# Kernel tuning notes

Hardware: AMD Instinct MI355X
Metric: run time of the kernel (lower is better)

Reference implementation:

```python
import math
import jax, jax.numpy as jnp
import numpy as np

B, S, D, H, HD = 2, 2048, 1024, 16, 64  # batch, seq, dim, heads, head_dim
EPS = 1e-5

def setup_inputs() -> dict:
    key = jax.random.key(0)
    ks = jax.random.split(key, 10)
    init = lambda k, shape: jax.random.normal(k, shape, jnp.float32) * 0.02
    return {
        "x": jax.random.normal(ks[0], (B, S, D), jnp.float32),
        "cos": jax.random.uniform(ks[1], (1, S, 1, 1, HD), dtype=jnp.float32),
        "sin": jax.random.uniform(ks[2], (1, S, 1, 1, HD), dtype=jnp.float32),
        "c": jax.random.normal(ks[3], (B, D), jnp.float32),
        "norm1_w": jnp.ones((D,), jnp.float32),
        "w_qkv": init(ks[4], (3 * D, D)),
        "w_out": init(ks[5], (D, D)),
        "norm2_w": jnp.ones((D,), jnp.float32),
        "mlp_w1": init(ks[6], (4 * D, D)),
        "mlp_b1": jnp.zeros((4 * D,), jnp.float32),
        "mlp_w2": init(ks[7], (D, 4 * D)),
        "mlp_b2": jnp.zeros((D,), jnp.float32),
        "ada_w": init(ks[8], (6 * D, D)),
        "ada_b": init(ks[9], (6 * D,)),
    }

def _ln(x, w):
    # LayerNorm computed in fp32, no bias, then scaled by weight
    xf = x.astype(jnp.float32)
    mu = xf.mean(-1, keepdims=True)
    var = xf.var(-1, keepdims=True)
    return (xf - mu) * jax.lax.rsqrt(var + EPS) * w

def _modulate(h, shift, scale):
    return h * (1.0 + scale[:, None, :]) + shift[:, None, :]

def reference(x, cos, sin, c, norm1_w, w_qkv, w_out, norm2_w,
              mlp_w1, mlp_b1, mlp_w2, mlp_b2, ada_w, ada_b):
    # adaLN modulation params: [B, 6D] -> six [B, D] chunks
    ada = c @ ada_w.T + ada_b
    sh_msa, sc_msa, g_msa, sh_mlp, sc_mlp, g_mlp = jnp.split(ada, 6, axis=-1)

    # attention branch (flash_attn path: no rotary applied, naive full softmax)
    h = _modulate(_ln(x, norm1_w), sh_msa, sc_msa)
    qkv = (h @ w_qkv.T).reshape(B, S, 3, H, HD)
    q, k, v = qkv[:, :, 0], qkv[:, :, 1], qkv[:, :, 2]
    scores = jnp.einsum('bqhd,bkhd->bhqk', q, k) / math.sqrt(HD)
    probs = jax.nn.softmax(scores, axis=-1)
    attn = jnp.einsum('bhqk,bkhd->bqhd', probs, v).reshape(B, S, D)
    # gate * dropout(out) + residual; eval mode -> dropout = identity
    x = x + g_msa[:, None, :] * (attn @ w_out.T)

    # MLP branch
    h = _modulate(_ln(x, norm2_w), sh_mlp, sc_mlp)
    h = jax.nn.gelu(h @ mlp_w1.T + mlp_b1, approximate=True) @ mlp_w2.T + mlp_b2
    return x + g_mlp[:, None, :] * h
```

## Files before the change

### kernel.cpp

```cpp
#include <hip/hip_runtime.h>
#include <stdint.h>

typedef __attribute__((ext_vector_type(4))) float f32x4;
typedef __attribute__((ext_vector_type(8))) __bf16 bf16x8;

#define DEV static __device__ __forceinline__

DEV unsigned short f2bf(float f){
    uint32_t u = __float_as_uint(f);
    u += 0x7FFFu + ((u >> 16) & 1u);
    return (unsigned short)(u >> 16);
}
DEV float bf2f(unsigned short s){
    uint32_t u = ((uint32_t)s) << 16;
    return __uint_as_float(u);
}

typedef __attribute__((address_space(1))) const void as1v;
typedef __attribute__((address_space(3))) void as3v;
DEV void g2l16(const void* g, void* l){
    __builtin_amdgcn_global_load_lds((as1v*)g, (as3v*)l, 16, 0, 0);
}

__global__ __launch_bounds__(256) void k_cast_bf16(const float* __restrict__ in,
                                                   unsigned short* __restrict__ out, int n4){
    int i = blockIdx.x * 256 + threadIdx.x;
    if (i < n4){
        float4 v = ((const float4*)in)[i];
        ((ushort4*)out)[i] = make_ushort4(f2bf(v.x), f2bf(v.y), f2bf(v.z), f2bf(v.w));
    }
}

__global__ __launch_bounds__(256) void k_cast_bf16q(const float* __restrict__ in,
                                                    unsigned short* __restrict__ out,
                                                    int n4, int nq4){
    int i = blockIdx.x * 256 + threadIdx.x;
    if (i < n4){
        float4 v = ((const float4*)in)[i];
        float s = (i < nq4) ? 0.18033688011112043f : 1.f;
        ((ushort4*)out)[i] = make_ushort4(f2bf(v.x * s), f2bf(v.y * s), f2bf(v.z * s), f2bf(v.w * s));
    }
}

__global__ __launch_bounds__(256) void k_ada(const float* __restrict__ c,
                                             const float* __restrict__ aw,
                                             const float* __restrict__ ab,
                                             float* __restrict__ out){
    int wid  = blockIdx.x * 4 + (threadIdx.x >> 6);
    int lane = threadIdx.x & 63;
    int b = wid / 6144, r = wid % 6144;
    const float4* cw = (const float4*)(c + (size_t)b * 1024);
    const float4* wr = (const float4*)(aw + (size_t)r * 1024);
    float s = 0.f;
    #pragma unroll
    for (int i = 0; i < 4; i++){
        float4 a = wr[lane + i * 64];
        float4 q = cw[lane + i * 64];
        s += a.x*q.x + a.y*q.y + a.z*q.z + a.w*q.w;
    }
    #pragma unroll
    for (int off = 32; off > 0; off >>= 1) s += __shfl_down(s, off);
    if (lane == 0) out[wid] = s + ab[r];
}

__global__ __launch_bounds__(256) void k_ln_mod(const float* __restrict__ x,
                                                const float* __restrict__ w,
                                                const float* __restrict__ ada,
                                                int sh_off, int sc_off,
                                                unsigned short* __restrict__ out){
    int row = blockIdx.x;
    int b   = row >> 11;
    int tid = threadIdx.x;
    float4 v = ((const float4*)(x + (size_t)row * 1024))[tid];
    float s  = v.x + v.y + v.z + v.w;
    float ss = v.x*v.x + v.y*v.y + v.z*v.z + v.w*v.w;
    #pragma unroll
    for (int off = 32; off > 0; off >>= 1){ s += __shfl_down(s, off); ss += __shfl_down(ss, off); }
    __shared__ float red[8];
    int wv = tid >> 6;
    if ((tid & 63) == 0){ red[wv] = s; red[4 + wv] = ss; }
    __syncthreads();
    float S  = red[0] + red[1] + red[2] + red[3];
    float SS = red[4] + red[5] + red[6] + red[7];
    float mu   = S * (1.f / 1024.f);
    float rstd = rsqrtf(SS * (1.f / 1024.f) - mu * mu + 1e-5f);
    const float* adab = ada + (size_t)b * 6144;
    float4 wv4 = ((const float4*)w)[tid];
    float4 sh  = ((const float4*)(adab + sh_off))[tid];
    float4 sc  = ((const float4*)(adab + sc_off))[tid];
    float h0 = (v.x - mu) * rstd * wv4.x * (1.f + sc.x) + sh.x;
    float h1 = (v.y - mu) * rstd * wv4.y * (1.f + sc.y) + sh.y;
    float h2 = (v.z - mu) * rstd * wv4.z * (1.f + sc.z) + sh.z;
    float h3 = (v.w - mu) * rstd * wv4.w * (1.f + sc.w) + sh.w;
    ((ushort4*)(out + (size_t)row * 1024))[tid] = make_ushort4(f2bf(h0), f2bf(h1), f2bf(h2), f2bf(h3));
}

template<int MODE>
__global__ __launch_bounds__(256) void k_gemm(const unsigned short* __restrict__ A,
                                              const unsigned short* __restrict__ B,
                                              void* __restrict__ outp,
                                              const float* __restrict__ bias,
                                              const float* __restrict__ res,
                                              const float* __restrict__ ada, int goff,
                                              int M, int N, int K){
    __shared__ unsigned short As[2 * 128 * 32];
    __shared__ unsigned short Bs[2 * 128 * 32];
    int tid = threadIdx.x, lane = tid & 63, wv = tid >> 6;
    int quad = lane >> 4, l15 = lane & 15;
    int wm = wv & 1, wn = wv >> 1;
    int bm = blockIdx.x, bn = blockIdx.y;
    int klo, khi;
    if constexpr (MODE == 3){
        klo = blockIdx.z * 1376;
        khi = klo + 1376; if (khi > K) khi = K;
    } else {
        klo = 0; khi = K;
    }
    f32x4 acc[4][4] = {};
    int srow = wv * 16 + (lane >> 2), sseg = lane & 3;
    const unsigned short* ga = A + (size_t)(bm * 128 + srow) * K + sseg * 8;
    const unsigned short* gb = B + (size_t)(bn * 128 + srow) * K + sseg * 8;
    size_t stride64 = (size_t)64 * K;
    int wb = wv * 512;
    g2l16(ga + klo,            As + wb);
    g2l16(ga + stride64 + klo, As + 2048 + wb);
    g2l16(gb + klo,            Bs + wb);
    g2l16(gb + stride64 + klo, Bs + 2048 + wb);
    for (int k0 = klo; k0 < khi; k0 += 32){
        int cur = ((k0 - klo) >> 5) & 1;
        unsigned short* as = As + cur * 4096;
        unsigned short* bs = Bs + cur * 4096;
        __syncthreads();
        if (k0 + 32 < khi){
            unsigned short* an = As + (cur ^ 1) * 4096;
            unsigned short* bn2 = Bs + (cur ^ 1) * 4096;
            g2l16(ga + k0 + 32,            an + wb);
            g2l16(ga + stride64 + k0 + 32, an + 2048 + wb);
            g2l16(gb + k0 + 32,            bn2 + wb);
            g2l16(gb + stride64 + k0 + 32, bn2 + 2048 + wb);
        }
        bf16x8 af[4], bfr[4];
        #pragma unroll
        for (int i = 0; i < 4; i++)
            af[i] = *(const bf16x8*)(as + (wm * 64 + i * 16 + l15) * 32 + quad * 8);
        #pragma unroll
        for (int j = 0; j < 4; j++)
            bfr[j] = *(const bf16x8*)(bs + (wn * 64 + j * 16 + l15) * 32 + quad * 8);
        #pragma unroll
        for (int i = 0; i < 4; i++)
            #pragma unroll
            for (int j = 0; j < 4; j++)
                acc[i][j] = __builtin_amdgcn_mfma_f32_16x16x32_bf16(af[i], bfr[j], acc[i][j], 0, 0, 0);
    }
    unsigned short* zp = nullptr;
    if constexpr (MODE == 3){
        int z = blockIdx.z;
        if (z < 2) zp = (unsigned short*)outp + (size_t)z * 4194304;
        else       zp = (unsigned short*)(void*)bias;
    }
    int row0 = bm * 128 + wm * 64, col0 = bn * 128 + wn * 64;
    #pragma unroll
    for (int i = 0; i < 4; i++){
        #pragma unroll
        for (int r = 0; r < 4; r++){
            int row = row0 + i * 16 + quad * 4 + r;
            #pragma unroll
            for (int j = 0; j < 4; j++){
                int col = col0 + j * 16 + l15;
                float v = acc[i][j][r];
                size_t idx = (size_t)row * N + col;
                if constexpr (MODE == 0){
                    ((unsigned short*)outp)[idx] = f2bf(v);
                } else if constexpr (MODE == 1){
                    float t = v + bias[col];
                    float u = 1.5957691216057308f * (t + 0.044715f * t * t * t);
                    float g = t / (1.f + __expf(-u));
                    ((unsigned short*)outp)[idx] = f2bf(g);
                } else if constexpr (MODE == 2){
                    float t = v;
                    if (bias) t += bias[col];
                    int bb = row >> 11;
                    float g = ada[(size_t)bb * 6144 + goff + col];
                    ((float*)outp)[idx] = res[idx] + g * t;
                } else {
                    zp[idx] = f2bf(v);
                }
            }
        }
    }
}

__global__ __launch_bounds__(256) void k_ep2(const unsigned short* __restrict__ z01,
                                             const unsigned short* __restrict__ z2,
                                             const float* __restrict__ bias,
                                             const float* __restrict__ res,
                                             const float* __restrict__ ada, int goff,
                                             float* __restrict__ out){
    int row = blockIdx.x;
    int bb  = row >> 11;
    int tid = threadIdx.x;
    size_t base = (size_t)row * 1024 + tid * 4;
    ushort4 a0 = *(const ushort4*)(z01 + base);
    ushort4 a1 = *(const ushort4*)(z01 + 4194304 + base);
    ushort4 a2 = *(const ushort4*)(z2 + base);
    float4 rv = *(const float4*)(res + base);
    float4 bv = ((const float4*)bias)[tid];
    float4 gv = ((const float4*)(ada + (size_t)bb * 6144 + goff))[tid];
    float4 o;
    o.x = rv.x + gv.x * (bf2f(a0.x) + bf2f(a1.x) + bf2f(a2.x) + bv.x);
    o.y = rv.y + gv.y * (bf2f(a0.y) + bf2f(a1.y) + bf2f(a2.y) + bv.y);
    o.z = rv.z + gv.z * (bf2f(a0.z) + bf2f(a1.z) + bf2f(a2.z) + bv.z);
    o.w = rv.w + gv.w * (bf2f(a0.w) + bf2f(a1.w) + bf2f(a2.w) + bv.w);
    *(float4*)(out + base) = o;
}

__global__ __launch_bounds__(256) void k_vt(const unsigned short* __restrict__ qkv,
                                            unsigned short* __restrict__ vt){
    __shared__ unsigned short T[64 * 66];
    int kb = blockIdx.x, bh = blockIdx.y;
    int b = bh >> 4, h = bh & 15;
    size_t rb = (size_t)b * 2048;
    int t = threadIdx.x;
    int key = t >> 2, seg = t & 3;
    const unsigned short* src = qkv + (rb + kb * 64 + key) * 3072 + 2048 + h * 64;
    uint4 v0 = *(const uint4*)(src + seg * 8);
    uint4 v1 = *(const uint4*)(src + 32 + seg * 8);
    const unsigned short* p0 = (const unsigned short*)&v0;
    const unsigned short* p1 = (const unsigned short*)&v1;
    unsigned short* tr = T + key * 66;
    ushort2* t0 = (ushort2*)(tr + seg * 8);
    ushort2* t1 = (ushort2*)(tr + 32 + seg * 8);
    #pragma unroll
    for (int j = 0; j < 4; j++){
        t0[j] = make_ushort2(p0[2*j], p0[2*j+1]);
        t1[j] = make_ushort2(p1[2*j], p1[2*j+1]);
    }
    __syncthreads();
    int d = t >> 2, kseg = t & 3;
    unsigned short obuf[16];
    #pragma unroll
    for (int j = 0; j < 16; j++) obuf[j] = T[(kseg * 16 + j) * 66 + d];
    uint4* dst = (uint4*)(vt + ((size_t)bh * 64 + d) * 2048 + kb * 64 + kseg * 16);
    dst[0] = ((const uint4*)obuf)[0];
    dst[1] = ((const uint4*)obuf)[1];
}

__global__ __launch_bounds__(256) void k_attn(const unsigned short* __restrict__ qkv,
                                              const unsigned short* __restrict__ vt,
                                              unsigned short* __restrict__ oh,
                                              float* __restrict__ lsb){
    __shared__ unsigned short Ks[2 * 4096];
    __shared__ unsigned short Vs[2 * 4096];
    __shared__ __align__(16) unsigned short Ps[4 * 32 * 72];
    int tid = threadIdx.x, lane = tid & 63, wv = tid >> 6;
    int quad = lane >> 4, l15 = lane & 15;
    int qt = blockIdx.x, bh = blockIdx.y, kvh = blockIdx.z;
    int b = bh >> 4, h = bh & 15;
    size_t rb = (size_t)b * 2048;
    int klo2 = kvh << 10, kend = klo2 + 1024;

    bf16x8 qb[2][2];
    #pragma unroll
    for (int t = 0; t < 2; t++){
        int qrow = qt * 128 + wv * 32 + t * 16 + l15;
        const unsigned short* qp = qkv + ((rb + qrow) * 3072 + h * 64 + quad * 8);
        qb[t][0] = *(const bf16x8*)qp;
        qb[t][1] = *(const bf16x8*)(qp + 32);
    }
    bf16x8 ONES;
    #pragma unroll
    for (int i = 0; i < 8; i++) ONES[i] = (__bf16)1.0f;
    f32x4 ls[2] = {};
    f32x4 o[2][4];
    #pragma unroll
    for (int t = 0; t < 2; t++)
        #pragma unroll
        for (int dt = 0; dt < 4; dt++) o[t][dt] = (f32x4){0.f, 0.f, 0.f, 0.f};

    int rr = wv * 16 + (lane >> 2), cs = lane & 3;
    const unsigned short* gk = qkv + (rb + rr) * 3072 + 1024 + h * 64 + cs * 8;
    const unsigned short* gv = vt + ((size_t)bh * 64 + rr) * 2048 + cs * 8;
    int soff = rr * 32 + (cs ^ ((rr >> 1) & 3)) * 8;
    int rsl = (quad ^ ((l15 >> 1) & 3)) * 8;
    unsigned short* Pw = Ps + wv * 32 * 72;

    uint4 rk0 = *(const uint4*)(gk + (size_t)klo2 * 3072);
    uint4 rk1 = *(const uint4*)(gk + (size_t)klo2 * 3072 + 32);
    uint4 rv0 = *(const uint4*)(gv + klo2);
    uint4 rv1 = *(const uint4*)(gv + klo2 + 32);

    for (int k0 = klo2; k0 < kend; k0 += 64){
        unsigned short* ks = Ks + ((k0 >> 6) & 1) * 4096;
        unsigned short* vs = Vs + ((k0 >> 6) & 1) * 4096;
        int kn = (k0 + 64 < kend) ? (k0 + 64) : k0;
        uint4 nk0 = *(const uint4*)(gk + (size_t)kn * 3072);
        uint4 nk1 = *(const uint4*)(gk + (size_t)kn * 3072 + 32);
        uint4 nv0 = *(const uint4*)(gv + kn);
        uint4 nv1 = *(const uint4*)(gv + kn + 32);
        *(uint4*)(ks + soff)        = rk0;
        *(uint4*)(ks + 2048 + soff) = rk1;
        *(uint4*)(vs + soff)        = rv0;
        *(uint4*)(vs + 2048 + soff) = rv1;
        __syncthreads();
        rk0 = nk0; rk1 = nk1; rv0 = nv0; rv1 = nv1;
        f32x4 c[2][4];
        #pragma unroll
        for (int kt = 0; kt < 4; kt++){
            bf16x8 ka0 = *(const bf16x8*)(ks + (kt * 16 + l15) * 32 + rsl);
            bf16x8 ka1 = *(const bf16x8*)(ks + 2048 + (kt * 16 + l15) * 32 + rsl);
            #pragma unroll
            for (int t = 0; t < 2; t++){
                f32x4 z = (f32x4){0.f, 0.f, 0.f, 0.f};
                z = __builtin_amdgcn_mfma_f32_16x16x32_bf16(ka0, qb[t][0], z, 0, 0, 0);
                z = __builtin_amdgcn_mfma_f32_16x16x32_bf16(ka1, qb[t][1], z, 0, 0, 0);
                c[t][kt] = z;
            }
        }
        #pragma unroll
        for (int t = 0; t < 2; t++){
            #pragma unroll
            for (int kt = 0; kt < 4; kt++){
                float p0 = __builtin_amdgcn_exp2f(c[t][kt][0]);
                float p1 = __builtin_amdgcn_exp2f(c[t][kt][1]);
                float p2 = __builtin_amdgcn_exp2f(c[t][kt][2]);
                float p3 = __builtin_amdgcn_exp2f(c[t][kt][3]);
                union { uint2 u; __bf16 bh4[4]; } w;
                w.bh4[0] = (__bf16)p0;
                w.bh4[1] = (__bf16)p1;
                w.bh4[2] = (__bf16)p2;
                w.bh4[3] = (__bf16)p3;
                *(uint2*)(Pw + (t * 16 + l15) * 72 + kt * 16 + quad * 4) = w.u;
            }
        }
        bf16x8 pa[2][2];
        #pragma unroll
        for (int t = 0; t < 2; t++){
            pa[t][0] = *(const bf16x8*)(Pw + (t * 16 + l15) * 72 + quad * 8);
            pa[t][1] = *(const bf16x8*)(Pw + (t * 16 + l15) * 72 + 32 + quad * 8);
        }
        #pragma unroll
        for (int t = 0; t < 2; t++){
            ls[t] = __builtin_amdgcn_mfma_f32_16x16x32_bf16(pa[t][0], ONES, ls[t], 0, 0, 0);
            ls[t] = __builtin_amdgcn_mfma_f32_16x16x32_bf16(pa[t][1], ONES, ls[t], 0, 0, 0);
        }
        #pragma unroll
        for (int dt = 0; dt < 4; dt++){
            bf16x8 vb0 = *(const bf16x8*)(vs + (dt * 16 + l15) * 32 + rsl);
            bf16x8 vb1 = *(const bf16x8*)(vs + 2048 + (dt * 16 + l15) * 32 + rsl);
            #pragma unroll
            for (int t = 0; t < 2; t++){
                o[t][dt] = __builtin_amdgcn_mfma_f32_16x16x32_bf16(pa[t][0], vb0, o[t][dt], 0, 0, 0);
                o[t][dt] = __builtin_amdgcn_mfma_f32_16x16x32_bf16(pa[t][1], vb1, o[t][dt], 0, 0, 0);
            }
        }
    }
    unsigned short* ohh = oh + (size_t)kvh * 4194304;
    float* lsh = lsb + (size_t)kvh * 65536;
    #pragma unroll
    for (int t = 0; t < 2; t++){
        #pragma unroll
        for (int r = 0; r < 4; r++){
            int row = qt * 128 + wv * 32 + t * 16 + quad * 4 + r;
            size_t grow = rb + row;
            unsigned short* op = ohh + (grow * 1024 + h * 64);
            #pragma unroll
            for (int dt = 0; dt < 4; dt++)
                op[dt * 16 + l15] = f2bf(o[t][dt][r]);
            if (l15 == 0) lsh[grow * 16 + h] = ls[t][r];
        }
    }
}

__global__ __launch_bounds__(256) void k_cmb(const unsigned short* __restrict__ oh,
                                             const float* __restrict__ lsb,
                                             unsigned short* __restrict__ out){
    int row = blockIdx.x;
    int tid = threadIdx.x;
    int col = tid * 4;
    int h = col >> 6;
    size_t base = (size_t)row * 1024 + col;
    ushort4 a = *(const ushort4*)(oh + base);
    ushort4 b = *(const ushort4*)(oh + 4194304 + base);
    float inv = 1.f / (lsb[row * 16 + h] + lsb[65536 + row * 16 + h]);
    ushort4 o;
    o.x = f2bf((bf2f(a.x) + bf2f(b.x)) * inv);
    o.y = f2bf((bf2f(a.y) + bf2f(b.y)) * inv);
    o.z = f2bf((bf2f(a.z) + bf2f(b.z)) * inv);
    o.w = f2bf((bf2f(a.w) + bf2f(b.w)) * inv);
    *(ushort4*)(out + base) = o;
}

extern "C" void kernel_launch(void* const* d_in, const int* in_sizes, int n_in,
                              void* d_out, int out_size, void* d_ws, size_t ws_size,
                              hipStream_t stream){
    const float* x     = (const float*)d_in[0];
    const float* c     = (const float*)d_in[3];
    const float* n1w   = (const float*)d_in[4];
    const float* w_qkv = (const float*)d_in[5];
    const float* w_out = (const float*)d_in[6];
    const float* n2w   = (const float*)d_in[7];
    const float* w1    = (const float*)d_in[8];
    const float* b1    = (const float*)d_in[9];
    const float* w2    = (const float*)d_in[10];
    const float* b2    = (const float*)d_in[11];
    const float* ada_w = (const float*)d_in[12];
    const float* ada_b = (const float*)d_in[13];
    float* out = (float*)d_out;
    char* ws = (char*)d_ws;

    unsigned short* wqkv_b = (unsigned short*)(ws + 0);
    unsigned short* wout_b = (unsigned short*)(ws + 6291456);
    unsigned short* w1_b   = (unsigned short*)(ws + 8388608);
    unsigned short* w2_b   = (unsigned short*)(ws + 16777216);
    float*          ada    = (float*)         (ws + 25165824);
    unsigned short* h      = (unsigned short*)(ws + 25214976);
    unsigned short* qkv    = (unsigned short*)(ws + 33603584);
    unsigned short* attn   = (unsigned short*)(ws + 58769408);
    float*          xn     = (float*)         (ws + 67158016);
    unsigned short* u      = qkv;
    unsigned short* vt     = h;
    unsigned short* oh  = (unsigned short*)(ws + 67158016);
    float*          lsb = (float*)         (ws + 0);
    unsigned short* z01 = (unsigned short*)(ws + 0);
    unsigned short* z2  = (unsigned short*)(ws + 25214976);

    k_cast_bf16q<<<3072, 256, 0, stream>>>(w_qkv, wqkv_b, 786432, 262144);
    k_cast_bf16<<<1024, 256, 0, stream>>>(w_out, wout_b,  262144);
    k_cast_bf16<<<4096, 256, 0, stream>>>(w1,    w1_b,   1048576);
    k_cast_bf16<<<4096, 256, 0, stream>>>(w2,    w2_b,   1048576);
    k_ada<<<3072, 256, 0, stream>>>(c, ada_w, ada_b, ada);
    k_ln_mod<<<4096, 256, 0, stream>>>(x, n1w, ada, 0, 1024, h);
    k_gemm<0><<<dim3(32, 24), 256, 0, stream>>>(h, wqkv_b, qkv, nullptr, nullptr, nullptr, 0, 4096, 3072, 1024);
    k_vt<<<dim3(32, 32), 256, 0, stream>>>(qkv, vt);
    k_attn<<<dim3(16, 32, 2), 256, 0, stream>>>(qkv, vt, oh, lsb);
    k_cmb<<<4096, 256, 0, stream>>>(oh, lsb, attn);
    k_gemm<2><<<dim3(32, 8), 256, 0, stream>>>(attn, wout_b, xn, nullptr, x, ada, 2048, 4096, 1024, 1024);
    k_ln_mod<<<4096, 256, 0, stream>>>(xn, n2w, ada, 3072, 4096, h);
    k_gemm<1><<<dim3(32, 32), 256, 0, stream>>>(h, w1_b, u, b1, nullptr, nullptr, 0, 4096, 4096, 1024);
    k_gemm<3><<<dim3(32, 8, 3), 256, 0, stream>>>(u, w2_b, z01, (const float*)z2, nullptr,
                                                  nullptr, 0, 4096, 1024, 4096);
    k_ep2<<<4096, 256, 0, stream>>>(z01, z2, b2, xn, ada, 5120, out);
}
```

Baseline: 402.6 us.

## Add triple-buffered 256x128 GEMM kernel for MLP up-projection

Adds a new 512-thread GEMM kernel with a 256x128 block tile and a three-stage LDS ring. Global-to-LDS loads for tile t+2 are interleaved with the MFMA work on tile t, using raised wave priority around the MFMA bursts. The kernel replaces the old 256-thread GEMM for the GELU-fused MLP first layer, aiming to hide load latency and raise arithmetic intensity. The trade-off is more LDS per block (about 144 KB) and fewer resident blocks, so occupancy drops.

```diff
diff --git a/kernel.cpp b/kernel.cpp
--- a/kernel.cpp
+++ b/kernel.cpp
@@ -190,6 +190,112 @@
     }
 }
 
+template<int MODE>
+__global__ __launch_bounds__(512) void k_gemm3(const unsigned short* __restrict__ A,
+                                               const unsigned short* __restrict__ B,
+                                               void* __restrict__ outp,
+                                               const float* __restrict__ bias,
+                                               int M, int N, int K){
+    __shared__ unsigned short S[3 * 24576];
+    int tid = threadIdx.x, lane = tid & 63, wid = tid >> 6;
+    int quad = lane >> 4, l15 = lane & 15;
+    int wm = wid >> 1, wn = wid & 1;
+    int bm = blockIdx.x, bn = blockIdx.y;
+    int wv8  = wid * 8;
+    int lrow = lane >> 3;
+    int ksw  = (lane & 7) ^ lrow;
+    int wmr = wm * 64, wnr = wn * 64;
+    int rsw = l15 & 7;
+
+    f32x4 acc[4][4] = {};
+    int nt = K >> 6;
+
+    auto STG = [&](int s, int kt, int part){
+        int k0 = kt << 6;
+        unsigned short* base = S + s * 24576;
+        if (part < 4){
+            const unsigned short* g = A + (size_t)(bm * 256 + part * 64 + wv8 + lrow) * K + k0 + ksw * 8;
+            g2l16(g, base + (part * 64 + wv8) * 64);
+        } else {
+            int c = part - 4;
+            const unsigned short* g = B + (size_t)(bn * 128 + c * 64 + wv8 + lrow) * K + k0 + ksw * 8;
+            g2l16(g, base + 16384 + (c * 64 + wv8) * 64);
+        }
+    };
+    #pragma unroll
+    for (int p = 0; p < 6; p++) STG(0, 0, p);
+    #pragma unroll
+    for (int p = 0; p < 6; p++) STG(1, 1, p);
+
+    for (int t = 0; t < nt; ++t){
+        int r = t % 3, s = (t + 2) % 3;
+        bool st = (t + 2) < nt;
+        if (t == nt - 1) asm volatile("s_waitcnt vmcnt(0)" ::: "memory");
+        else             asm volatile("s_waitcnt vmcnt(6)" ::: "memory");
+        __builtin_amdgcn_s_barrier();
+        __builtin_amdgcn_sched_barrier(0);
+        const unsigned short* buf = S + r * 24576;
+        bf16x8 bfr[4][2];
+        #pragma unroll
+        for (int j = 0; j < 4; j++){
+            int R = wnr + j * 16 + l15;
+            bfr[j][0] = *(const bf16x8*)(buf + 16384 + R * 64 + ((0 * 4 + quad) ^ rsw) * 8);
+            bfr[j][1] = *(const bf16x8*)(buf + 16384 + R * 64 + ((1 * 4 + quad) ^ rsw) * 8);
+        }
+        int R0 = wmr + l15;
+        bf16x8 a0 = *(const bf16x8*)(buf + R0 * 64 + ((0 * 4 + quad) ^ rsw) * 8);
+        bf16x8 a1 = *(const bf16x8*)(buf + R0 * 64 + ((1 * 4 + quad) ^ rsw) * 8);
+        if (st){ STG(s, t + 2, 0); STG(s, t + 2, 1); }
+        asm volatile("s_waitcnt lgkmcnt(0)" ::: "memory");
+        __builtin_amdgcn_sched_barrier(0);
+        __builtin_amdgcn_s_setprio(1);
+        #pragma unroll
+        for (int j = 0; j < 4; j++){
+            acc[0][j] = __builtin_amdgcn_mfma_f32_16x16x32_bf16(a0, bfr[j][0], acc[0][j], 0, 0, 0);
+            acc[0][j] = __builtin_amdgcn_mfma_f32_16x16x32_bf16(a1, bfr[j][1], acc[0][j], 0, 0, 0);
+        }
+        __builtin_amdgcn_s_setprio(0);
+        #pragma unroll
+        for (int i = 1; i < 4; i++){
+            int Ri = wmr + i * 16 + l15;
+            a0 = *(const bf16x8*)(buf + Ri * 64 + ((0 * 4 + quad) ^ rsw) * 8);
+            a1 = *(const bf16x8*)(buf + Ri * 64 + ((1 * 4 + quad) ^ rsw) * 8);
+            if (st && i < 3){ STG(s, t + 2, 2 * i); STG(s, t + 2, 2 * i + 1); }
+            asm volatile("s_waitcnt lgkmcnt(0)" ::: "memory");
+            __builtin_amdgcn_sched_barrier(0);
+            __builtin_amdgcn_s_setprio(1);
+            #pragma unroll
+            for (int j = 0; j < 4; j++){
+                acc[i][j] = __builtin_amdgcn_mfma_f32_16x16x32_bf16(a0, bfr[j][0], acc[i][j], 0, 0, 0);
+                acc[i][j] = __builtin_amdgcn_mfma_f32_16x16x32_bf16(a1, bfr[j][1], acc[i][j], 0, 0, 0);
+            }
+            __builtin_amdgcn_s_setprio(0);
+        }
+    }
+    int row0 = bm * 256 + wm * 64, col0 = bn * 128 + wn * 64;
+    #pragma unroll
+    for (int i = 0; i < 4; i++){
+        #pragma unroll
+        for (int r = 0; r < 4; r++){
+            int row = row0 + i * 16 + quad * 4 + r;
+            #pragma unroll
+            for (int j = 0; j < 4; j++){
+                int col = col0 + j * 16 + l15;
+                float v = acc[i][j][r];
+                size_t idx = (size_t)row * N + col;
+                if constexpr (MODE == 1){
+                    float t = v + bias[col];
+                    float u = 1.5957691216057308f * (t + 0.044715f * t * t * t);
+                    float g = t / (1.f + __expf(-u));
+                    ((unsigned short*)outp)[idx] = f2bf(g);
+                } else {
+                    ((unsigned short*)outp)[idx] = f2bf(v);
+                }
+            }
+        }
+    }
+}
+
 __global__ __launch_bounds__(256) void k_ep2(const unsigned short* __restrict__ z01,
                                              const unsigned short* __restrict__ z2,
                                              const float* __restrict__ bias,
@@ -436,7 +542,7 @@
     k_cmb<<<4096, 256, 0, stream>>>(oh, lsb, attn);
     k_gemm<2><<<dim3(32, 8), 256, 0, stream>>>(attn, wout_b, xn, nullptr, x, ada, 2048, 4096, 1024, 1024);
     k_ln_mod<<<4096, 256, 0, stream>>>(xn, n2w, ada, 3072, 4096, h);
-    k_gemm<1><<<dim3(32, 32), 256, 0, stream>>>(h, w1_b, u, b1, nullptr, nullptr, 0, 4096, 4096, 1024);
+    k_gemm3<1><<<dim3(16, 32), 512, 0, stream>>>(h, w1_b, u, b1, 4096, 4096, 1024);
     k_gemm<3><<<dim3(32, 8, 3), 256, 0, stream>>>(u, w2_b, z01, (const float*)z2, nullptr,
                                                   nullptr, 0, 4096, 1024, 4096);
     k_ep2<<<4096, 256, 0, stream>>>(z01, z2, b2, xn, ada, 5120, out);
```

Result: no change. 408.4 us (+1.4%).
